# Kernel tuning notes

Measured on AMD Instinct MI355X. Metric: run time of the kernel, lower is better.

## Reference

```python
import jax, jax.numpy as jnp
import numpy as np

N_NODES = 100000
NEG_SLOPE = 0.2


def gat_conv(x, W, att_src, att_dst, bias, src, dst, heads, out_ch):
    # x: [N, F_in]; W: [F_in, heads*out_ch]; att_*: [heads, out_ch]; bias: [heads*out_ch]
    N = x.shape[0]
    h = (x @ W).reshape(N, heads, out_ch)                 # [N, H, C]
    a_src = jnp.sum(h * att_src[None], axis=-1)           # [N, H]
    a_dst = jnp.sum(h * att_dst[None], axis=-1)           # [N, H]
    # per-edge unnormalized attention logits (PyG GATConv)
    alpha = jax.nn.leaky_relu(a_src[src] + a_dst[dst], NEG_SLOPE)   # [E, H]
    # scatter-softmax over edges grouped by destination node
    m = jax.ops.segment_max(alpha, dst, num_segments=N)   # [N, H]
    m = jnp.where(jnp.isfinite(m), m, 0.0)
    e = jnp.exp(alpha - m[dst])                           # [E, H]
    s = jax.ops.segment_sum(e, dst, num_segments=N)       # [N, H]
    alpha = e / (s[dst] + 1e-16)
    # weighted scatter-add aggregation of neighbor features
    out = jax.ops.segment_sum(alpha[:, :, None] * h[src], dst, num_segments=N)  # [N, H, C]
    return out.reshape(N, heads * out_ch) + bias


def setup_inputs() -> dict:
    key = jax.random.key(0)
    ks = jax.random.split(key, 10)
    F_in = 128
    x = jax.random.normal(ks[0], (N_NODES, F_in), dtype=jnp.float32)
    edge_index = jax.random.randint(ks[1], (2, 3200000), 0, N_NODES, dtype=jnp.int64)
    g = 0.1
    return {
        "x": x,
        "edge_index": edge_index,
        "W1": jax.random.normal(ks[2], (F_in, 32), jnp.float32) * g,
        "att_src1": jax.random.normal(ks[3], (2, 16), jnp.float32) * g,
        "att_dst1": jax.random.normal(ks[4], (2, 16), jnp.float32) * g,
        "b1": jnp.zeros((32,), jnp.float32),
        "W2": jax.random.normal(ks[5], (32, 2), jnp.float32) * g,
        "att_src2": jax.random.normal(ks[6], (1, 2), jnp.float32) * g,
        "att_dst2": jax.random.normal(ks[7], (1, 2), jnp.float32) * g,
        "b2": jnp.zeros((2,), jnp.float32),
    }


def reference(x, edge_index, W1, att_src1, att_dst1, b1, W2, att_src2, att_dst2, b2):
    N = x.shape[0]
    # add self-loops (PyG GATConv default add_self_loops=True)
    loops = jnp.arange(N, dtype=edge_index.dtype)
    src = jnp.concatenate([edge_index[0], loops])
    dst = jnp.concatenate([edge_index[1], loops])
    h = gat_conv(x, W1, att_src1, att_dst1, b1, src, dst, heads=2, out_ch=16)
    h = jax.nn.elu(h)
    h = gat_conv(h, W2, att_src2, att_dst2, b2, src, dst, heads=1, out_ch=2)
    return jax.nn.log_softmax(h, axis=1)
```

## Files before the change

### kernel.cpp

```cpp
#include <hip/hip_runtime.h>
#include <hip/hip_bf16.h>

#define LEAK  0.2f
#define NPB   200
#define CAP   8192
#define CAPSH 13
#define SBITS 17
#define SMASK 0x1FFFF
#define CHUNK 4096

__global__ __launch_bounds__(512) void kbin(const int* __restrict__ ei, int E, int K,
                                            int* __restrict__ cursor,
                                            int* __restrict__ binned) {
    __shared__ int hist[512], lo[512], gb[512], lc[512];
    __shared__ int2 stag[CHUNK];
    __shared__ int probe;
    int t = threadIdx.x;
    hist[t] = 0;
    if (t == 0) probe = 0;
    __syncthreads();
    if (t < 256) {
        int zc = 0;
#pragma unroll
        for (int j = 0; j < 4; j++) zc += (ei[(t * 4 + j) * 2 + 1] == 0) ? 1 : 0;
        if (zc) atomicAdd(&probe, zc);
    }
    __syncthreads();
    int f = (probe == 1024);
    int e0 = blockIdx.x * CHUNK;
    int ss[8], dd[8];
#pragma unroll
    for (int i = 0; i < 8; i++) {
        int e = e0 + t + 512 * i;
        ss[i] = -1;
        dd[i] = 0;
        if (e < E) {
            int s, d;
            if (f) { s = ei[2 * (long long)e]; d = ei[2 * ((long long)e + E)]; }
            else   { s = ei[e];                d = ei[(long long)e + E]; }
            ss[i] = s;
            dd[i] = d;
            atomicAdd(&hist[d / NPB], 1);
        }
    }
    __syncthreads();
    int v = hist[t], x = v;
    for (int o = 1; o < 512; o <<= 1) {
        int y = (t >= o) ? hist[t - o] : 0;
        __syncthreads();
        x += y;
        hist[t] = x;
        __syncthreads();
    }
    int tb = x - v;
    lo[t] = tb;
    lc[t] = tb;
    if (t < K && v) {
        int rel = atomicAdd(&cursor[t], v);
        gb[t] = (t << CAPSH) + rel;
    }
    __syncthreads();
#pragma unroll
    for (int i = 0; i < 8; i++) {
        if (ss[i] >= 0) {
            int bk = dd[i] / NPB;
            int pos = atomicAdd(&lc[bk], 1);
            stag[pos] = make_int2(ss[i], dd[i]);
        }
    }
    __syncthreads();
    int cnt = min(CHUNK, E - e0);
#pragma unroll
    for (int i = 0; i < 8; i++) {
        int idx = t + 512 * i;
        if (idx < cnt) {
            int2 sd2 = stag[idx];
            int bk = sd2.y / NPB;
            int dloc = sd2.y - bk * NPB;
            int gpos = gb[bk] + (idx - lo[bk]);
            if (gpos < ((bk + 1) << CAPSH))
                binned[gpos] = sd2.x | (dloc << SBITS);
        }
    }
}

__global__ __launch_bounds__(256) void k1(const float* __restrict__ x,
                                          const float* __restrict__ W1,
                                          const float* __restrict__ atts,
                                          const float* __restrict__ attd,
                                          float* __restrict__ h1,
                                          float* __restrict__ a1s,
                                          float* __restrict__ a1d, int N) {
    __shared__ float Ws[128 * 32];
    __shared__ float xs[64 * 132];
    int t = threadIdx.x;
    const float4* W4 = (const float4*)W1;
    float4* Ws4 = (float4*)Ws;
#pragma unroll
    for (int i = 0; i < 4; i++) Ws4[t + 256 * i] = W4[t + 256 * i];
    long long node0 = (long long)blockIdx.x * 64;
    const float4* x4 = (const float4*)x;
    float4* xs4 = (float4*)xs;
#pragma unroll
    for (int i = 0; i < 8; i++) {
        int idx = t + 256 * i;
        int row = idx >> 5, col = idx & 31;
        long long n = node0 + row;
        float4 v = make_float4(0.f, 0.f, 0.f, 0.f);
        if (n < N) v = x4[n * 32 + col];
        xs4[row * 33 + col] = v;
    }
    __syncthreads();

    int cg = t & 7, ns = t >> 3;
    const float4* xr0 = (const float4*)(xs + (ns * 2) * 132);
    const float4* xr1 = (const float4*)(xs + (ns * 2 + 1) * 132);
    float acc0[4] = {0.f, 0.f, 0.f, 0.f}, acc1[4] = {0.f, 0.f, 0.f, 0.f};
#pragma unroll 8
    for (int k4 = 0; k4 < 32; k4++) {
        float4 xa = xr0[k4], xb = xr1[k4];
        float av[4] = {xa.x, xa.y, xa.z, xa.w};
        float bv[4] = {xb.x, xb.y, xb.z, xb.w};
#pragma unroll
        for (int i = 0; i < 4; i++) {
            float4 w = Ws4[(k4 * 4 + i) * 8 + cg];
            acc0[0] = fmaf(av[i], w.x, acc0[0]);
            acc0[1] = fmaf(av[i], w.y, acc0[1]);
            acc0[2] = fmaf(av[i], w.z, acc0[2]);
            acc0[3] = fmaf(av[i], w.w, acc0[3]);
            acc1[0] = fmaf(bv[i], w.x, acc1[0]);
            acc1[1] = fmaf(bv[i], w.y, acc1[1]);
            acc1[2] = fmaf(bv[i], w.z, acc1[2]);
            acc1[3] = fmaf(bv[i], w.w, acc1[3]);
        }
    }
    long long gn0 = node0 + ns * 2, gn1 = gn0 + 1;
    float4* h14 = (float4*)h1;
    if (gn0 < N) h14[gn0 * 8 + cg] = make_float4(acc0[0], acc0[1], acc0[2], acc0[3]);
    if (gn1 < N) h14[gn1 * 8 + cg] = make_float4(acc1[0], acc1[1], acc1[2], acc1[3]);

    float ps0 = 0.f, pd0 = 0.f, ps1 = 0.f, pd1 = 0.f;
#pragma unroll
    for (int i = 0; i < 4; i++) {
        float aa = atts[cg * 4 + i], dd = attd[cg * 4 + i];
        ps0 = fmaf(acc0[i], aa, ps0);
        pd0 = fmaf(acc0[i], dd, pd0);
        ps1 = fmaf(acc1[i], aa, ps1);
        pd1 = fmaf(acc1[i], dd, pd1);
    }
#pragma unroll
    for (int m = 1; m < 4; m <<= 1) {
        ps0 += __shfl_xor(ps0, m, 64);
        pd0 += __shfl_xor(pd0, m, 64);
        ps1 += __shfl_xor(ps1, m, 64);
        pd1 += __shfl_xor(pd1, m, 64);
    }
    if ((cg & 3) == 0) {
        int hd = cg >> 2;
        if (gn0 < N) { a1s[gn0 * 2 + hd] = ps0; a1d[gn0 * 2 + hd] = pd0; }
        if (gn1 < N) { a1s[gn1 * 2 + hd] = ps1; a1d[gn1 * 2 + hd] = pd1; }
    }
}

__global__ __launch_bounds__(512) void kfused(const int* __restrict__ cursor,
                                              const int* __restrict__ binned,
                                              const float* __restrict__ h1,
                                              const float* __restrict__ a1s,
                                              const float* __restrict__ a1d,
                                              const float* __restrict__ b1,
                                              const float* __restrict__ W2,
                                              const float* __restrict__ as2,
                                              const float* __restrict__ ad2,
                                              float4* __restrict__ pk,
                                              int* __restrict__ srcs,
                                              int* __restrict__ off,
                                              int* __restrict__ deg, int N) {
    __shared__ int lsrc[CAP];
    __shared__ int ldeg[NPB], lcur[NPB], loff[NPB];
    __shared__ int sd[512];
    int b = blockIdx.x, t = threadIdx.x;
    int node0 = b * NPB;
    int nn = min(NPB, N - node0);
    int cnt = cursor[b];
    if (cnt > CAP) cnt = CAP;
    const int* bb = binned + ((long long)b << CAPSH);
    if (t < NPB) ldeg[t] = 0;
    __syncthreads();
    for (int i = t; i < cnt; i += 512) atomicAdd(&ldeg[bb[i] >> SBITS], 1);
    __syncthreads();
    int v = (t < nn) ? ldeg[t] : 0, x = v;
    sd[t] = x;
    __syncthreads();
    for (int o = 1; o < 512; o <<= 1) {
        int y = (t >= o) ? sd[t - o] : 0;
        __syncthreads();
        x += y;
        sd[t] = x;
        __syncthreads();
    }
    if (t < nn) {
        int rel = x - v;
        loff[t] = rel;
        lcur[t] = rel;
        off[node0 + t] = (b << CAPSH) + rel;
        deg[node0 + t] = v;
    }
    __syncthreads();
    for (int i = t; i < cnt; i += 512) {
        int p = bb[i];
        int pos = atomicAdd(&lcur[p >> SBITS], 1);
        lsrc[pos] = p & SMASK;
    }
    __syncthreads();
    for (int i = t; i < cnt; i += 512) srcs[((long long)b << CAPSH) + i] = lsrc[i];

    int wv = t >> 6, lane = t & 63;
    int e8 = lane >> 3, c4 = lane & 7, hd = c4 >> 2;
    bool wlane = (c4 & 3) == 0;
    const float4* h14 = (const float4*)h1;
    for (int ni = wv; ni < nn; ni += 8) {
        int n = node0 + ni;
        float a1dn = a1d[2 * n + hd];
        int base = loff[ni], g = ldeg[ni];
        float4 acc = make_float4(0.f, 0.f, 0.f, 0.f);
        float wsum = 0.f;
        for (int tt = e8 - 1; tt < g; tt += 8) {
            int s = (tt < 0) ? n : lsrc[base + tt];
            float al = a1s[2 * s + hd] + a1dn;
            al = al > 0.f ? al : LEAK * al;
            float w = __expf(al);
            float4 hv = h14[(size_t)s * 8 + c4];
            acc.x = fmaf(w, hv.x, acc.x);
            acc.y = fmaf(w, hv.y, acc.y);
            acc.z = fmaf(w, hv.z, acc.z);
            acc.w = fmaf(w, hv.w, acc.w);
            if (wlane) wsum += w;
        }
#pragma unroll
        for (int m = 8; m < 64; m <<= 1) {
            acc.x += __shfl_xor(acc.x, m, 64);
            acc.y += __shfl_xor(acc.y, m, 64);
            acc.z += __shfl_xor(acc.z, m, 64);
            acc.w += __shfl_xor(acc.w, m, 64);
            wsum += __shfl_xor(wsum, m, 64);
        }
        float wsH = __shfl(wsum, hd * 4, 64);
        float inv = 1.f / (wsH + 1e-16f);
        float4 bv = ((const float4*)b1)[c4];
        float4 t1;
        t1.x = acc.x * inv + bv.x;
        t1.y = acc.y * inv + bv.y;
        t1.z = acc.z * inv + bv.z;
        t1.w = acc.w * inv + bv.w;
        t1.x = t1.x > 0.f ? t1.x : __expf(t1.x) - 1.f;
        t1.y = t1.y > 0.f ? t1.y : __expf(t1.y) - 1.f;
        t1.z = t1.z > 0.f ? t1.z : __expf(t1.z) - 1.f;
        t1.w = t1.w > 0.f ? t1.w : __expf(t1.w) - 1.f;
        const float4* W24 = (const float4*)W2;
        float4 wA = W24[c4 * 2], wB = W24[c4 * 2 + 1];
        float p0 = t1.x * wA.x + t1.y * wA.z + t1.z * wB.x + t1.w * wB.z;
        float p1 = t1.x * wA.y + t1.y * wA.w + t1.z * wB.y + t1.w * wB.w;
#pragma unroll
        for (int m = 1; m < 8; m <<= 1) {
            p0 += __shfl_xor(p0, m, 64);
            p1 += __shfl_xor(p1, m, 64);
        }
        if (lane == 0)
            pk[n] = make_float4(p0 * as2[0] + p1 * as2[1], p0, p1,
                                p0 * ad2[0] + p1 * ad2[1]);
    }
}

__global__ __launch_bounds__(256) void kagg2(const int* __restrict__ off,
                                             const int* __restrict__ deg,
                                             const int* __restrict__ srcs,
                                             const float4* __restrict__ pk,
                                             const float* __restrict__ b2,
                                             float* __restrict__ out, int N) {
    int wv = threadIdx.x >> 6;
    int lane = threadIdx.x & 63;
    int n = blockIdx.x * 4 + wv;
    if (n >= N) return;
    float adn = pk[n].w;
    int base = off[n], g = deg[n];
    float a0 = 0.f, a1v = 0.f, ws = 0.f;
    for (int t = lane - 1; t < g; t += 64) {
        int s = (t < 0) ? n : srcs[base + t];
        float4 p = pk[s];
        float al = p.x + adn;
        al = al > 0.f ? al : LEAK * al;
        float w = __expf(al);
        a0 = fmaf(w, p.y, a0);
        a1v = fmaf(w, p.z, a1v);
        ws += w;
    }
#pragma unroll
    for (int m = 1; m < 64; m <<= 1) {
        a0 += __shfl_xor(a0, m, 64);
        a1v += __shfl_xor(a1v, m, 64);
        ws += __shfl_xor(ws, m, 64);
    }
    if (lane == 0) {
        float inv = 1.f / (ws + 1e-16f);
        float o0 = a0 * inv + b2[0];
        float o1 = a1v * inv + b2[1];
        float mx = fmaxf(o0, o1);
        float lse = mx + __logf(__expf(o0 - mx) + __expf(o1 - mx));
        out[2 * n] = o0 - lse;
        out[2 * n + 1] = o1 - lse;
    }
}

extern "C" void kernel_launch(void* const* d_in, const int* in_sizes, int n_in,
                              void* d_out, int out_size, void* d_ws, size_t ws_size,
                              hipStream_t stream) {
    const float* x   = (const float*)d_in[0];
    const int*   ei  = (const int*)d_in[1];
    const float* W1  = (const float*)d_in[2];
    const float* as1 = (const float*)d_in[3];
    const float* ad1 = (const float*)d_in[4];
    const float* b1  = (const float*)d_in[5];
    const float* W2  = (const float*)d_in[6];
    const float* as2 = (const float*)d_in[7];
    const float* ad2 = (const float*)d_in[8];
    const float* b2  = (const float*)d_in[9];
    float* out = (float*)d_out;

    int N = out_size / 2;
    int E = in_sizes[1] / 2;
    int K = (N + NPB - 1) / NPB;

    float* ws    = (float*)d_ws;
    float* h1    = ws;
    float4* pk   = (float4*)(h1 + (size_t)N * 32);
    float* a1s   = (float*)(pk + (size_t)N);
    float* a1d   = a1s + (size_t)N * 2;
    int* deg     = (int*)(a1d + (size_t)N * 2);
    int* off     = deg + N;
    int* srcs    = off + N;
    int* binned  = srcs + (size_t)K * CAP;
    int* cursor  = binned + (size_t)K * CAP;

    int nblkE = (E + CHUNK - 1) / CHUNK;

    hipMemsetAsync(cursor, 0, K * sizeof(int), stream);
    kbin<<<nblkE, 512, 0, stream>>>(ei, E, K, cursor, binned);
    k1<<<(N + 63) / 64, 256, 0, stream>>>(x, W1, as1, ad1, h1, a1s, a1d, N);
    kfused<<<K, 512, 0, stream>>>(cursor, binned, h1, a1s, a1d,
                                  b1, W2, as2, ad2, pk, srcs, off, deg, N);
    kagg2<<<(N + 3) / 4, 256, 0, stream>>>(off, deg, srcs, pk, b2, out, N);
}
```

Measured before the change: 262.3 us.

## Store h1 in bf16 and precompute per-edge attention weights in shared memory

k1 now writes the layer-1 features as packed bf16, which halves the bytes of the gathered h1 rows. kfused computes each edge's exp-attention weight once, during the counting-sort scatter, rather than redundantly per lane in the aggregation loop. It accumulates the softmax denominators with shared atomics and stores self-loops explicitly in the CSR, which lets kagg2 drop its self-loop special case. The cost is bf16 rounding error on features and weights, extra shared memory (lwu) that may lower occupancy, and reserving NPB slots of capacity for self-loops.

```diff
diff --git a/kernel.cpp b/kernel.cpp
--- a/kernel.cpp
+++ b/kernel.cpp
@@ -8,6 +8,13 @@
 #define SBITS 17
 #define SMASK 0x1FFFF
 #define CHUNK 4096
+
+__device__ __forceinline__ unsigned pkbf(float a, float b) {
+    unsigned ua = __float_as_uint(a), ub = __float_as_uint(b);
+    ua += 0x7fff + ((ua >> 16) & 1);
+    ub += 0x7fff + ((ub >> 16) & 1);
+    return (ua >> 16) | (ub & 0xffff0000u);
+}
 
 __global__ __launch_bounds__(512) void kbin(const int* __restrict__ ei, int E, int K,
                                             int* __restrict__ cursor,
@@ -88,7 +95,7 @@
                                           const float* __restrict__ W1,
                                           const float* __restrict__ atts,
                                           const float* __restrict__ attd,
-                                          float* __restrict__ h1,
+                                          uint2* __restrict__ h1b,
                                           float* __restrict__ a1s,
                                           float* __restrict__ a1d, int N) {
     __shared__ float Ws[128 * 32];
@@ -135,9 +142,10 @@
         }
     }
     long long gn0 = node0 + ns * 2, gn1 = gn0 + 1;
-    float4* h14 = (float4*)h1;
-    if (gn0 < N) h14[gn0 * 8 + cg] = make_float4(acc0[0], acc0[1], acc0[2], acc0[3]);
-    if (gn1 < N) h14[gn1 * 8 + cg] = make_float4(acc1[0], acc1[1], acc1[2], acc1[3]);
+    if (gn0 < N) h1b[gn0 * 8 + cg] = make_uint2(pkbf(acc0[0], acc0[1]),
+                                                pkbf(acc0[2], acc0[3]));
+    if (gn1 < N) h1b[gn1 * 8 + cg] = make_uint2(pkbf(acc1[0], acc1[1]),
+                                                pkbf(acc1[2], acc1[3]));
 
     float ps0 = 0.f, pd0 = 0.f, ps1 = 0.f, pd1 = 0.f;
 #pragma unroll
@@ -164,7 +172,7 @@
 
 __global__ __launch_bounds__(512) void kfused(const int* __restrict__ cursor,
                                               const int* __restrict__ binned,
-                                              const float* __restrict__ h1,
+                                              const uint2* __restrict__ h1b,
                                               const float* __restrict__ a1s,
                                               const float* __restrict__ a1d,
                                               const float* __restrict__ b1,
@@ -176,19 +184,28 @@
                                               int* __restrict__ off,
                                               int* __restrict__ deg, int N) {
     __shared__ int lsrc[CAP];
+    __shared__ unsigned lwu[CAP];
     __shared__ int ldeg[NPB], lcur[NPB], loff[NPB];
+    __shared__ float lws[NPB * 2];
+    __shared__ float2 la1d[NPB];
     __shared__ int sd[512];
+    __shared__ int stot;
     int b = blockIdx.x, t = threadIdx.x;
     int node0 = b * NPB;
     int nn = min(NPB, N - node0);
     int cnt = cursor[b];
-    if (cnt > CAP) cnt = CAP;
+    if (cnt > CAP - NPB) cnt = CAP - NPB;
     const int* bb = binned + ((long long)b << CAPSH);
-    if (t < NPB) ldeg[t] = 0;
+    if (t < NPB) {
+        ldeg[t] = 0;
+        if (t < nn) la1d[t] = ((const float2*)a1d)[node0 + t];
+    }
     __syncthreads();
     for (int i = t; i < cnt; i += 512) atomicAdd(&ldeg[bb[i] >> SBITS], 1);
     __syncthreads();
-    int v = (t < nn) ? ldeg[t] : 0, x = v;
+    int v = (t < nn) ? ldeg[t] : 0;
+    int seg = (t < nn) ? v + 1 : 0;
+    int x = seg;
     sd[t] = x;
     __syncthreads();
     for (int o = 1; o < 512; o <<= 1) {
@@ -199,42 +216,62 @@
         __syncthreads();
     }
     if (t < nn) {
-        int rel = x - v;
+        int rel = x - seg;
         loff[t] = rel;
-        lcur[t] = rel;
+        lcur[t] = rel + 1;
         off[node0 + t] = (b << CAPSH) + rel;
-        deg[node0 + t] = v;
-    }
+        deg[node0 + t] = seg;
+        int n = node0 + t;
+        float2 as = ((const float2*)a1s)[n];
+        float2 ad = la1d[t];
+        float al0 = as.x + ad.x, al1 = as.y + ad.y;
+        al0 = al0 > 0.f ? al0 : LEAK * al0;
+        al1 = al1 > 0.f ? al1 : LEAK * al1;
+        float w0 = __expf(al0), w1 = __expf(al1);
+        lws[2 * t] = w0;
+        lws[2 * t + 1] = w1;
+        lsrc[rel] = n;
+        lwu[rel] = pkbf(w0, w1);
+    }
+    if (t == nn - 1) stot = x;
     __syncthreads();
     for (int i = t; i < cnt; i += 512) {
         int p = bb[i];
-        int pos = atomicAdd(&lcur[p >> SBITS], 1);
-        lsrc[pos] = p & SMASK;
-    }
-    __syncthreads();
-    for (int i = t; i < cnt; i += 512) srcs[((long long)b << CAPSH) + i] = lsrc[i];
+        int s = p & SMASK, dloc = p >> SBITS;
+        float2 as = ((const float2*)a1s)[s];
+        float2 ad = la1d[dloc];
+        float al0 = as.x + ad.x, al1 = as.y + ad.y;
+        al0 = al0 > 0.f ? al0 : LEAK * al0;
+        al1 = al1 > 0.f ? al1 : LEAK * al1;
+        float w0 = __expf(al0), w1 = __expf(al1);
+        atomicAdd(&lws[2 * dloc], w0);
+        atomicAdd(&lws[2 * dloc + 1], w1);
+        int pos = atomicAdd(&lcur[dloc], 1);
+        lsrc[pos] = s;
+        lwu[pos] = pkbf(w0, w1);
+    }
+    __syncthreads();
+    int tot = stot;
+    for (int i = t; i < tot; i += 512) srcs[((long long)b << CAPSH) + i] = lsrc[i];
 
     int wv = t >> 6, lane = t & 63;
     int e8 = lane >> 3, c4 = lane & 7, hd = c4 >> 2;
-    bool wlane = (c4 & 3) == 0;
-    const float4* h14 = (const float4*)h1;
     for (int ni = wv; ni < nn; ni += 8) {
-        int n = node0 + ni;
-        float a1dn = a1d[2 * n + hd];
-        int base = loff[ni], g = ldeg[ni];
+        int base = loff[ni], g = ldeg[ni] + 1;
         float4 acc = make_float4(0.f, 0.f, 0.f, 0.f);
-        float wsum = 0.f;
-        for (int tt = e8 - 1; tt < g; tt += 8) {
-            int s = (tt < 0) ? n : lsrc[base + tt];
-            float al = a1s[2 * s + hd] + a1dn;
-            al = al > 0.f ? al : LEAK * al;
-            float w = __expf(al);
-            float4 hv = h14[(size_t)s * 8 + c4];
-            acc.x = fmaf(w, hv.x, acc.x);
-            acc.y = fmaf(w, hv.y, acc.y);
-            acc.z = fmaf(w, hv.z, acc.z);
-            acc.w = fmaf(w, hv.w, acc.w);
-            if (wlane) wsum += w;
+        for (int tt = e8; tt < g; tt += 8) {
+            int s = lsrc[base + tt];
+            unsigned wp = lwu[base + tt];
+            float w = __uint_as_float(hd ? (wp & 0xffff0000u) : (wp << 16));
+            uint2 hb = h1b[(size_t)s * 8 + c4];
+            float h0 = __uint_as_float(hb.x << 16);
+            float h1v = __uint_as_float(hb.x & 0xffff0000u);
+            float h2 = __uint_as_float(hb.y << 16);
+            float h3 = __uint_as_float(hb.y & 0xffff0000u);
+            acc.x = fmaf(w, h0, acc.x);
+            acc.y = fmaf(w, h1v, acc.y);
+            acc.z = fmaf(w, h2, acc.z);
+            acc.w = fmaf(w, h3, acc.w);
         }
 #pragma unroll
         for (int m = 8; m < 64; m <<= 1) {
@@ -242,10 +279,8 @@
             acc.y += __shfl_xor(acc.y, m, 64);
             acc.z += __shfl_xor(acc.z, m, 64);
             acc.w += __shfl_xor(acc.w, m, 64);
-            wsum += __shfl_xor(wsum, m, 64);
-        }
-        float wsH = __shfl(wsum, hd * 4, 64);
-        float inv = 1.f / (wsH + 1e-16f);
+        }
+        float inv = 1.f / (lws[2 * ni + hd] + 1e-16f);
         float4 bv = ((const float4*)b1)[c4];
         float4 t1;
         t1.x = acc.x * inv + bv.x;
@@ -266,8 +301,8 @@
             p1 += __shfl_xor(p1, m, 64);
         }
         if (lane == 0)
-            pk[n] = make_float4(p0 * as2[0] + p1 * as2[1], p0, p1,
-                                p0 * ad2[0] + p1 * ad2[1]);
+            pk[node0 + ni] = make_float4(p0 * as2[0] + p1 * as2[1], p0, p1,
+                                         p0 * ad2[0] + p1 * ad2[1]);
     }
 }
 
@@ -284,8 +319,8 @@
     float adn = pk[n].w;
     int base = off[n], g = deg[n];
     float a0 = 0.f, a1v = 0.f, ws = 0.f;
-    for (int t = lane - 1; t < g; t += 64) {
-        int s = (t < 0) ? n : srcs[base + t];
+    for (int t = lane; t < g; t += 64) {
+        int s = srcs[base + t];
         float4 p = pk[s];
         float al = p.x + adn;
         al = al > 0.f ? al : LEAK * al;
@@ -331,9 +366,9 @@
     int K = (N + NPB - 1) / NPB;
 
     float* ws    = (float*)d_ws;
-    float* h1    = ws;
-    float4* pk   = (float4*)(h1 + (size_t)N * 32);
-    float* a1s   = (float*)(pk + (size_t)N);
+    float4* pk   = (float4*)ws;
+    uint2* h1b   = (uint2*)(pk + (size_t)N);
+    float* a1s   = (float*)(h1b + (size_t)N * 8);
     float* a1d   = a1s + (size_t)N * 2;
     int* deg     = (int*)(a1d + (size_t)N * 2);
     int* off     = deg + N;
@@ -345,8 +380,8 @@
 
     hipMemsetAsync(cursor, 0, K * sizeof(int), stream);
     kbin<<<nblkE, 512, 0, stream>>>(ei, E, K, cursor, binned);
-    k1<<<(N + 63) / 64, 256, 0, stream>>>(x, W1, as1, ad1, h1, a1s, a1d, N);
-    kfused<<<K, 512, 0, stream>>>(cursor, binned, h1, a1s, a1d,
+    k1<<<(N + 63) / 64, 256, 0, stream>>>(x, W1, as1, ad1, h1b, a1s, a1d, N);
+    kfused<<<K, 512, 0, stream>>>(cursor, binned, h1b, a1s, a1d,
                                   b1, W2, as2, ad2, pk, srcs, off, deg, N);
     kagg2<<<(N + 3) / 4, 256, 0, stream>>>(off, deg, srcs, pk, b2, out, N);
 }
```

Measured after the change: 298.4 us. 1.14x slower.
